# Kernel optimization log

Measured on AMD Instinct MI355X. Metric: run time of the kernel, lower is better.

## Reference

```python
import jax, jax.numpy as jnp
import numpy as np
from jax import lax

SCALE = 2
K_UP = 5
BN_EPS = 1e-5
DN = ('NCHW', 'OIHW', 'NCHW')


def bn_eval(x, gamma, beta):
    # BatchNorm2d in eval mode with running_mean=0, running_var=1
    s = gamma / jnp.sqrt(1.0 + BN_EPS)
    return x * s[None, :, None, None] + beta[None, :, None, None]


def pixel_shuffle(x, r):
    b, C, h, w = x.shape
    c = C // (r * r)
    x = x.reshape(b, c, r, r, h, w)
    x = x.transpose(0, 1, 4, 2, 5, 3)  # b, c, h, r, w, r
    return x.reshape(b, c, h * r, w * r)


def setup_inputs() -> dict:
    key = jax.random.key(0)
    ks = jax.random.split(key, 3)
    b, c, h, w = 4, 128, 64, 64
    c_mid = 64
    return {
        'X': jax.random.normal(ks[0], (b, c, h, w), dtype=jnp.float32),
        'comp_w': jax.random.normal(ks[1], (c_mid, c, 1, 1), dtype=jnp.float32) * 0.05,
        'comp_g': jnp.ones((c_mid,), jnp.float32),
        'comp_b': jnp.zeros((c_mid,), jnp.float32),
        'enc_w': jax.random.normal(ks[2], ((SCALE * K_UP) ** 2, c_mid, 3, 3), dtype=jnp.float32) * 0.05,
        'enc_g': jnp.ones(((SCALE * K_UP) ** 2,), jnp.float32),
        'enc_b': jnp.zeros(((SCALE * K_UP) ** 2,), jnp.float32),
    }


def reference(X, comp_w, comp_g, comp_b, enc_w, enc_g, enc_b):
    b, c, h, w = X.shape
    h_, w_ = h * SCALE, w * SCALE
    pad = K_UP // 2 * SCALE  # = 4

    # comp: 1x1 conv + BN + SiLU
    W = lax.conv_general_dilated(X, comp_w, (1, 1), [(0, 0), (0, 0)], dimension_numbers=DN)
    W = jax.nn.silu(bn_eval(W, comp_g, comp_b))
    # enc: 3x3 conv (pad 1) + BN, no activation
    W = lax.conv_general_dilated(W, enc_w, (1, 1), [(1, 1), (1, 1)], dimension_numbers=DN)
    W = bn_eval(W, enc_g, enc_b)
    # pixel shuffle -> [b, k_up^2, h_, w_], softmax over kernel dim
    W = pixel_shuffle(W, SCALE)
    W = jax.nn.softmax(W, axis=1)

    # nearest-neighbor upsample of X
    Xu = jnp.repeat(jnp.repeat(X, SCALE, axis=2), SCALE, axis=3)  # [b, c, h_, w_]
    # unfold: kernel k_up, dilation=scale, padding=pad (im2col, channel-major)
    P = lax.conv_general_dilated_patches(
        Xu, (K_UP, K_UP), (1, 1), [(pad, pad), (pad, pad)],
        rhs_dilation=(SCALE, SCALE), dimension_numbers=DN)  # [b, c*k^2, h_, w_]
    P = P.reshape(b, c, K_UP * K_UP, h_, w_)

    return jnp.einsum('bkhw,bckhw->bchw', W, P)
```

## Files before the change

### kernel.cpp

```cpp
#include <hip/hip_runtime.h>
#include <hip/hip_bf16.h>
#include <math.h>

#define Bn   4
#define CIN  128
#define Hh   64
#define Ww   64
#define HW   4096
#define CMID 64
#define KOC  100
#define H2   128
#define W2d  128
#define HW2  16384
#define KUP  5
#define BN_EPS 1e-5f
#define CCH  8

typedef __attribute__((ext_vector_type(4)))  short  short4v;
typedef __attribute__((ext_vector_type(8)))  short  short8v;
typedef __attribute__((ext_vector_type(4)))  float  float4v;
typedef __attribute__((ext_vector_type(16))) float  float16v;

__device__ __forceinline__ ushort f2bf(float v) {
    __hip_bfloat16 h = __float2bfloat16(v);
    return *(ushort*)&h;
}
__device__ __forceinline__ float bfbits2f(ushort u) {
    unsigned x = ((unsigned)u) << 16;
    return __uint_as_float(x);
}

__global__ __launch_bounds__(256) void comp_kernel(
    const float* __restrict__ X,
    const float* __restrict__ cw,
    const float* __restrict__ cg,
    const float* __restrict__ cb,
    const float* __restrict__ ew,
    ushort* __restrict__ W1b,
    ushort* __restrict__ Abf)
{
    int tid = threadIdx.x;
    int bid = blockIdx.x;

    if (tid < 72) {
        int i   = bid * 72 + tid;
        int cm  = i & 63;
        int kop = (i >> 6) & 127;
        int tap = i >> 13;
        float v = (kop < KOC) ? ew[((size_t)(kop * CMID + cm)) * 9 + tap] : 0.f;
        Abf[i] = f2bf(v);
    }

    int b    = bid >> 8;
    int rem  = bid & 255;
    int pixG = rem >> 1;
    int coH  = rem & 1;

    int lane = tid & 63;
    int wid  = tid >> 6;
    int i16  = lane & 15;
    int u    = lane >> 4;

    int co0  = coH * 32 + (wid >> 1) * 16;
    int pix  = pixG * 32 + (wid & 1) * 16 + i16;

    const float* xcol = X  + (size_t)b * CIN * HW + pix;
    const float* arow = cw + (size_t)(co0 + i16) * CIN;

    float4v acc;
    acc[0] = 0.f; acc[1] = 0.f; acc[2] = 0.f; acc[3] = 0.f;

#pragma unroll
    for (int c = 0; c < 4; ++c) {
        int k0 = c * 32 + u * 8;
        float4 wa0 = *(const float4*)(arow + k0);
        float4 wa1 = *(const float4*)(arow + k0 + 4);
        float wv[8] = {wa0.x, wa0.y, wa0.z, wa0.w, wa1.x, wa1.y, wa1.z, wa1.w};
        float xv[8];
#pragma unroll
        for (int e = 0; e < 8; ++e)
            xv[e] = xcol[(size_t)(k0 + e) * HW];

        short8v ah, al, bh, bl;
#pragma unroll
        for (int e = 0; e < 8; ++e) {
            ushort h = f2bf(wv[e]);
            ah[e] = (short)h;
            al[e] = (short)f2bf(wv[e] - bfbits2f(h));
            ushort xh = f2bf(xv[e]);
            bh[e] = (short)xh;
            bl[e] = (short)f2bf(xv[e] - bfbits2f(xh));
        }
        acc = __builtin_amdgcn_mfma_f32_16x16x32_bf16(ah, bh, acc, 0, 0, 0);
        acc = __builtin_amdgcn_mfma_f32_16x16x32_bf16(ah, bl, acc, 0, 0, 0);
        acc = __builtin_amdgcn_mfma_f32_16x16x32_bf16(al, bh, acc, 0, 0, 0);
    }

    float inv_s = rsqrtf(1.0f + BN_EPS);
    int cob = co0 + u * 4;
    float4 gg = *(const float4*)(cg + cob);
    float4 bb = *(const float4*)(cb + cob);
    float v0 = acc[0] * (gg.x * inv_s) + bb.x;
    float v1 = acc[1] * (gg.y * inv_s) + bb.y;
    float v2 = acc[2] * (gg.z * inv_s) + bb.z;
    float v3 = acc[3] * (gg.w * inv_s) + bb.w;
    v0 = v0 / (1.f + expf(-v0));
    v1 = v1 / (1.f + expf(-v1));
    v2 = v2 / (1.f + expf(-v2));
    v3 = v3 / (1.f + expf(-v3));
    short4v pk;
    pk[0] = (short)f2bf(v0); pk[1] = (short)f2bf(v1);
    pk[2] = (short)f2bf(v2); pk[3] = (short)f2bf(v3);
    *(short4v*)(W1b + ((size_t)b * HW + pix) * 64 + cob) = pk;
}

__global__ __launch_bounds__(256) void enc_kernel(
    const ushort* __restrict__ W1b_us,
    const ushort* __restrict__ Abf,
    const float* __restrict__ eg,
    const float* __restrict__ eb,
    float* __restrict__ Wsm)
{
    __shared__ ushort Bs[3 * 34 * 72];
    __shared__ float  redm[4][8][32];
    __shared__ float  reds[4][8][32];

    int bid   = blockIdx.x;
    int whalf = bid & 1;
    int h     = (bid >> 1) & 63;
    int b     = bid >> 7;
    int w0    = whalf * 32;
    int tid   = threadIdx.x;

    const unsigned* src  = (const unsigned*)W1b_us;
    unsigned*       dstu = (unsigned*)Bs;
    for (int i = tid; i < 3 * 34 * 32; i += 256) {
        int cp = i & 31;
        int t  = i >> 5;
        int wl = t % 34;
        int r  = t / 34;
        int gr = h - 1 + r, gw = w0 - 1 + wl;
        unsigned val = 0u;
        if ((unsigned)gr < 64u && (unsigned)gw < 64u)
            val = src[((size_t)b * HW + gr * 64 + gw) * 32 + cp];
        dstu[(r * 34 + wl) * 36 + cp] = val;
    }
    __syncthreads();

    int lane = tid & 63;
    int wid  = tid >> 6;
    int n    = lane & 31;
    int q    = lane >> 5;

    float16v acc;
#pragma unroll
    for (int i = 0; i < 16; ++i) acc[i] = 0.f;

    const ushort* Arow = Abf + ((size_t)(wid * 32 + n)) * 64 + q * 8;

#pragma unroll
    for (int tap = 0; tap < 9; ++tap) {
        int dy = tap / 3, dx = tap % 3;
        int bbase = ((dy * 34) + n + dx) * 72 + q * 8;
        const ushort* Atap = Arow + (size_t)tap * 128 * 64;
#pragma unroll
        for (int c = 0; c < 4; ++c) {
            short8v a = *(const short8v*)(Atap + c * 16);
            short8v bf = *(const short8v*)(Bs + bbase + c * 16);
            acc = __builtin_amdgcn_mfma_f32_32x32x16_bf16(a, bf, acc, 0, 0, 0);
        }
    }

    float inv_s = rsqrtf(1.0f + BN_EPS);
    int   widq  = wid * 2 + q;

    float v[16];
    float pmax[4] = {-1e30f, -1e30f, -1e30f, -1e30f};
#pragma unroll
    for (int g = 0; g < 4; ++g) {
        int base = wid * 32 + 8 * g + 4 * q;
        if (base < KOC) {
            float4 gg = *(const float4*)(eg + base);
            float4 bb = *(const float4*)(eb + base);
            float v0 = acc[4*g+0] * (gg.x * inv_s) + bb.x;
            float v1 = acc[4*g+1] * (gg.y * inv_s) + bb.y;
            float v2 = acc[4*g+2] * (gg.z * inv_s) + bb.z;
            float v3 = acc[4*g+3] * (gg.w * inv_s) + bb.w;
            v[4*g+0] = v0; v[4*g+1] = v1; v[4*g+2] = v2; v[4*g+3] = v3;
            pmax[0] = fmaxf(pmax[0], v0);
            pmax[1] = fmaxf(pmax[1], v1);
            pmax[2] = fmaxf(pmax[2], v2);
            pmax[3] = fmaxf(pmax[3], v3);
        } else {
            v[4*g+0] = -1e30f; v[4*g+1] = -1e30f;
            v[4*g+2] = -1e30f; v[4*g+3] = -1e30f;
        }
    }

#pragma unroll
    for (int j = 0; j < 4; ++j) redm[j][widq][n] = pmax[j];
    __syncthreads();
    float m[4];
#pragma unroll
    for (int j = 0; j < 4; ++j) {
        float mm = redm[j][0][n];
#pragma unroll
        for (int i = 1; i < 8; ++i) mm = fmaxf(mm, redm[j][i][n]);
        m[j] = mm;
    }

    float psum[4] = {0.f, 0.f, 0.f, 0.f};
#pragma unroll
    for (int g = 0; g < 4; ++g) {
#pragma unroll
        for (int j = 0; j < 4; ++j) {
            float e = expf(v[4*g+j] - m[j]);
            v[4*g+j] = e;
            psum[j] += e;
        }
    }
#pragma unroll
    for (int j = 0; j < 4; ++j) reds[j][widq][n] = psum[j];
    __syncthreads();
    float inv[4];
#pragma unroll
    for (int j = 0; j < 4; ++j) {
        float ss = reds[j][0][n];
#pragma unroll
        for (int i = 1; i < 8; ++i) ss += reds[j][i][n];
        inv[j] = 1.f / ss;
    }

    int pixn = h * 64 + w0 + n;
    float* Wp = Wsm + ((size_t)b * 25 * HW + pixn) * 4;
#pragma unroll
    for (int g = 0; g < 4; ++g) {
        int k = wid * 8 + 2 * g + q;
        if (k < 25) {
            float4 st = make_float4(v[4*g+0] * inv[0], v[4*g+1] * inv[1],
                                    v[4*g+2] * inv[2], v[4*g+3] * inv[3]);
            *(float4*)(Wp + (size_t)k * HW * 4) = st;
        }
    }
}

__global__ __launch_bounds__(256) void carafe_kernel(
    const float* __restrict__ X,
    const float* __restrict__ Wsm,
    float* __restrict__ out)
{
    int gt = blockIdx.x * blockDim.x + threadIdx.x;
    int w  = gt & 63;
    int h  = (gt >> 6) & 63;
    int b  = (gt >> 12) & 3;
    int chunk = gt >> 14;
    int c0 = chunk * CCH;
    int pix = h * Ww + w;

    float wt[100];
    const float* wpb = Wsm + ((size_t)b * 25 * HW + pix) * 4;
#pragma unroll
    for (int k = 0; k < 25; ++k) {
        float4 wv = *(const float4*)(wpb + (size_t)k * HW * 4);
        wt[k]      = wv.x;
        wt[25 + k] = wv.y;
        wt[50 + k] = wv.z;
        wt[75 + k] = wv.w;
    }

    int off[25];
#pragma unroll
    for (int ki = 0; ki < 5; ++ki) {
#pragma unroll
        for (int kj = 0; kj < 5; ++kj) {
            int k = ki * 5 + kj;
            int r = h + ki - 2, cc = w + kj - 2;
            bool valid = ((unsigned)r < 64u) && ((unsigned)cc < 64u);
            int rc = r < 0 ? 0 : (r > 63 ? 63 : r);
            int cx = cc < 0 ? 0 : (cc > 63 ? 63 : cc);
            off[k] = rc * Ww + cx;
            if (!valid) { wt[k] = 0.f; wt[25+k] = 0.f; wt[50+k] = 0.f; wt[75+k] = 0.f; }
        }
    }

    const float* xp = X + ((size_t)b * CIN + c0) * HW;
    float* o0 = out + ((size_t)b * CIN + c0) * HW2 + (2 * h) * W2d + 2 * w;

    for (int c = 0; c < CCH; ++c) {
        float x[25];
#pragma unroll
        for (int k = 0; k < 25; ++k) x[k] = xp[off[k]];
        float a0 = 0.f, a1 = 0.f, a2 = 0.f, a3 = 0.f;
#pragma unroll
        for (int k = 0; k < 25; ++k) {
            float xv = x[k];
            a0 += wt[k]      * xv;
            a1 += wt[25 + k] * xv;
            a2 += wt[50 + k] * xv;
            a3 += wt[75 + k] * xv;
        }
        *(float2*)o0          = make_float2(a0, a1);
        *(float2*)(o0 + W2d)  = make_float2(a2, a3);
        xp += HW;
        o0 += HW2;
    }
}

extern "C" void kernel_launch(void* const* d_in, const int* in_sizes, int n_in,
                              void* d_out, int out_size, void* d_ws, size_t ws_size,
                              hipStream_t stream)
{
    const float* X  = (const float*)d_in[0];
    const float* cw = (const float*)d_in[1];
    const float* cg = (const float*)d_in[2];
    const float* cb = (const float*)d_in[3];
    const float* ew = (const float*)d_in[4];
    const float* eg = (const float*)d_in[5];
    const float* eb = (const float*)d_in[6];
    float* out = (float*)d_out;

    char* ws = (char*)d_ws;
    ushort* W1b = (ushort*)ws;
    ushort* Abf = (ushort*)(ws + 2097152);
    float*  Wsm = (float*)(ws + 2097152 + 147456);

    comp_kernel  <<<1024, 256, 0, stream>>>(X, cw, cg, cb, ew, W1b, Abf);
    enc_kernel   <<<512, 256, 0, stream>>>(W1b, Abf, eg, eb, Wsm);
    carafe_kernel<<<16 * Bn * HW / 256, 256, 0, stream>>>(X, Wsm, out);
}
```

Before: 117.4 us.

## Restructure CARAFE loop to stream weights per tap and halve channels per thread

The CARAFE kernel no longer holds all 100 softmax weights in registers. It now loads each tap's float4 weight inside the tap loop and accumulates across 4 channels, where before it used 8. This cuts register pressure so occupancy can rise, and the grid doubles to cover all 128 channels. In exchange each weight is reloaded once per thread across twice as many threads, which raises weight traffic.

New measurement: 126.0 us. 1.07x slower.

```diff
diff --git a/kernel.cpp b/kernel.cpp
--- a/kernel.cpp
+++ b/kernel.cpp
@@ -14,7 +14,7 @@
 #define HW2  16384
 #define KUP  5
 #define BN_EPS 1e-5f
-#define CCH  8
+#define CCH2 4
 
 typedef __attribute__((ext_vector_type(4)))  short  short4v;
 typedef __attribute__((ext_vector_type(8)))  short  short8v;
@@ -254,21 +254,18 @@
     int h  = (gt >> 6) & 63;
     int b  = (gt >> 12) & 3;
     int chunk = gt >> 14;
-    int c0 = chunk * CCH;
+    int c0 = chunk * CCH2;
     int pix = h * Ww + w;
 
-    float wt[100];
     const float* wpb = Wsm + ((size_t)b * 25 * HW + pix) * 4;
-#pragma unroll
-    for (int k = 0; k < 25; ++k) {
-        float4 wv = *(const float4*)(wpb + (size_t)k * HW * 4);
-        wt[k]      = wv.x;
-        wt[25 + k] = wv.y;
-        wt[50 + k] = wv.z;
-        wt[75 + k] = wv.w;
-    }
-
-    int off[25];
+    const float* xp0 = X + ((size_t)b * CIN + c0) * HW;
+
+    float acc[CCH2][4];
+#pragma unroll
+    for (int c = 0; c < CCH2; ++c) {
+        acc[c][0] = 0.f; acc[c][1] = 0.f; acc[c][2] = 0.f; acc[c][3] = 0.f;
+    }
+
 #pragma unroll
     for (int ki = 0; ki < 5; ++ki) {
 #pragma unroll
@@ -278,30 +275,27 @@
             bool valid = ((unsigned)r < 64u) && ((unsigned)cc < 64u);
             int rc = r < 0 ? 0 : (r > 63 ? 63 : r);
             int cx = cc < 0 ? 0 : (cc > 63 ? 63 : cc);
-            off[k] = rc * Ww + cx;
-            if (!valid) { wt[k] = 0.f; wt[25+k] = 0.f; wt[50+k] = 0.f; wt[75+k] = 0.f; }
-        }
-    }
-
-    const float* xp = X + ((size_t)b * CIN + c0) * HW;
+            int off = rc * Ww + cx;
+
+            float4 wv = *(const float4*)(wpb + (size_t)k * HW * 4);
+            if (!valid) { wv.x = 0.f; wv.y = 0.f; wv.z = 0.f; wv.w = 0.f; }
+
+#pragma unroll
+            for (int c = 0; c < CCH2; ++c) {
+                float xv = xp0[(size_t)c * HW + off];
+                acc[c][0] += wv.x * xv;
+                acc[c][1] += wv.y * xv;
+                acc[c][2] += wv.z * xv;
+                acc[c][3] += wv.w * xv;
+            }
+        }
+    }
+
     float* o0 = out + ((size_t)b * CIN + c0) * HW2 + (2 * h) * W2d + 2 * w;
-
-    for (int c = 0; c < CCH; ++c) {
-        float x[25];
-#pragma unroll
-        for (int k = 0; k < 25; ++k) x[k] = xp[off[k]];
-        float a0 = 0.f, a1 = 0.f, a2 = 0.f, a3 = 0.f;
-#pragma unroll
-        for (int k = 0; k < 25; ++k) {
-            float xv = x[k];
-            a0 += wt[k]      * xv;
-            a1 += wt[25 + k] * xv;
-            a2 += wt[50 + k] * xv;
-            a3 += wt[75 + k] * xv;
-        }
-        *(float2*)o0          = make_float2(a0, a1);
-        *(float2*)(o0 + W2d)  = make_float2(a2, a3);
-        xp += HW;
+#pragma unroll
+    for (int c = 0; c < CCH2; ++c) {
+        *(float2*)o0         = make_float2(acc[c][0], acc[c][1]);
+        *(float2*)(o0 + W2d) = make_float2(acc[c][2], acc[c][3]);
         o0 += HW2;
     }
 }
@@ -326,5 +320,5 @@
 
     comp_kernel  <<<1024, 256, 0, stream>>>(X, cw, cg, cb, ew, W1b, Abf);
     enc_kernel   <<<512, 256, 0, stream>>>(W1b, Abf, eg, eb, Wsm);
-    carafe_kernel<<<16 * Bn * HW / 256, 256, 0, stream>>>(X, Wsm, out);
-}
+    carafe_kernel<<<2048, 256, 0, stream>>>(X, Wsm, out);
+}
```
